# Performance work log

Measured on AMD Instinct MI355X. Metric: run time of the kernel, lower is better.

The kernel has to match this reference:

```python
import jax, jax.numpy as jnp
import numpy as np

D_MODEL = 1024
NHEAD = 8
DPH = D_MODEL // NHEAD
DFF = 2048
EPS = 1e-5


def _layernorm(x, w, b):
    mu = jnp.mean(x, axis=-1, keepdims=True)
    var = jnp.mean((x - mu) ** 2, axis=-1, keepdims=True)
    return (x - mu) / jnp.sqrt(var + EPS) * w + b


def setup_inputs() -> dict:
    key = jax.random.key(0)
    ks = jax.random.split(key, 8)
    B, L = 8, 2048
    x = jax.random.normal(ks[0], (B, L, D_MODEL), dtype=jnp.float32)
    # HeadWiseLinear: per-head weight (nhead, dph, 4*dph), bias (nhead, 4*dph)
    ih_w = jax.random.normal(ks[1], (NHEAD, DPH, 4 * DPH), dtype=jnp.float32) * (1.0 / np.sqrt(DPH))
    # forget-gate bias init: linspace(3,6,d_model) in the f slot (second chunk), zeros elsewhere
    init_vals = jnp.linspace(3.0, 6.0, D_MODEL, dtype=jnp.float32).reshape(NHEAD, 1, DPH)
    init_vals = jnp.pad(init_vals, ((0, 0), (1, 2), (0, 0)))  # rows: i, f, z, o
    ih_b = init_vals.reshape(NHEAD, 4 * DPH)
    # linear_hh: Linear(dph, 4*dph, bias=False), stored as (dph, 4*dph) (x @ W)
    hh_w = jax.random.normal(ks[2], (DPH, 4 * DPH), dtype=jnp.float32) * (1.0 / np.sqrt(DPH))
    ln1_w = jnp.ones((D_MODEL,), jnp.float32); ln1_b = jnp.zeros((D_MODEL,), jnp.float32)
    ln2_w = jnp.ones((D_MODEL,), jnp.float32); ln2_b = jnp.zeros((D_MODEL,), jnp.float32)
    hn_w = jnp.ones((DPH,), jnp.float32); hn_b = jnp.zeros((DPH,), jnp.float32)
    ff_w1 = jax.random.normal(ks[3], (D_MODEL, 2 * DFF), dtype=jnp.float32) * (1.0 / np.sqrt(D_MODEL))
    ff_b1 = jnp.zeros((2 * DFF,), jnp.float32)
    ff_w2 = jax.random.normal(ks[4], (DFF, D_MODEL), dtype=jnp.float32) * (1.0 / np.sqrt(DFF))
    ff_b2 = jnp.zeros((D_MODEL,), jnp.float32)
    return dict(x=x, ih_w=ih_w, ih_b=ih_b, hh_w=hh_w, ln1_w=ln1_w, ln1_b=ln1_b,
                hn_w=hn_w, hn_b=hn_b, ln2_w=ln2_w, ln2_b=ln2_b,
                ff_w1=ff_w1, ff_b1=ff_b1, ff_w2=ff_w2, ff_b2=ff_b2)


def _slstm_core(x, ih_w, ih_b, hh_w, hn_w, hn_b):
    B, L, D = x.shape
    xh = x.reshape(B, L, NHEAD, DPH)
    # headwise input projection: (B,L,H,4*dph)
    proj = jnp.einsum('blhd,hdf->blhf', xh, ih_w) + ih_b
    proj = jnp.transpose(proj, (1, 0, 2, 3))  # (L,B,H,4*dph)

    h0 = jnp.zeros((B, NHEAD, DPH), x.dtype)
    c0 = jnp.zeros_like(h0)
    m0 = jnp.full_like(h0, -jnp.inf)  # stabilizer; matches scalar-0 first-step semantics
    n0 = jnp.zeros_like(h0)

    def step(carry, p_t):
        h, c, m, n = carry
        p = p_t + jnp.einsum('bhd,df->bhf', h, hh_w)
        i, f, z, o = jnp.split(p, 4, axis=-1)
        z = jnp.tanh(z)
        o = jax.nn.sigmoid(o)
        f = jax.nn.log_sigmoid(f) + m
        m_new = jnp.maximum(f, i)
        i_s = jnp.exp(i - m_new)
        f_s = jnp.exp(f - m_new)
        c = f_s * c + i_s * z
        n = f_s * n + i_s
        h = o * (c / n)
        return (h, c, m_new, n), h

    (h, c, _, _), out = jax.lax.scan(step, (h0, c0, m0, n0), proj)
    out = jnp.transpose(out, (1, 0, 2, 3))  # (B,L,H,dph)
    out = _layernorm(out, hn_w, hn_b)
    return out.reshape(B, L, D), (h, c)


def reference(x, ih_w, ih_b, hh_w, ln1_w, ln1_b, hn_w, hn_b, ln2_w, ln2_b,
              ff_w1, ff_b1, ff_w2, ff_b2):
    core_out, _ = _slstm_core(_layernorm(x, ln1_w, ln1_b), ih_w, ih_b, hh_w, hn_w, hn_b)
    y = core_out + x
    z = _layernorm(y, ln2_w, ln2_b)
    x12 = z @ ff_w1 + ff_b1
    x1, x2 = jnp.split(x12, 2, axis=-1)
    ff = (x1 * jax.nn.gelu(x2, approximate=False)) @ ff_w2 + ff_b2
    return ff + y
```

## Files before the change

### kernel.cpp

```cpp
#include <hip/hip_runtime.h>
#include <math.h>


#define D_MODEL 1024
#define NHEAD   8
#define DPH     128
#define DFF     2048
#define BATCH   8
#define SEQ     2048
#define NROWS   (BATCH * SEQ)
#define CHUNK_L 256
#define TGRP    16
#define NGRP    (CHUNK_L / TGRP)
#define ROWCH   4096
#define LN_EPS  1e-5f

typedef __attribute__((ext_vector_type(8))) short short8;
typedef __attribute__((ext_vector_type(4))) short short4v;
typedef __attribute__((ext_vector_type(4))) float f32x4;
typedef __attribute__((ext_vector_type(2))) _Float16 h2f;
typedef __attribute__((ext_vector_type(8))) _Float16 h8f;
union H8U { h8f v; h2f p[4]; };

#if __has_builtin(__builtin_amdgcn_fdot2)
#define DOT2(a, b, c) __builtin_amdgcn_fdot2((a), (b), (c), false)
#else
__device__ __forceinline__ float DOT2(h2f a, h2f b, float c) {
  return c + (float)a.x * (float)b.x + (float)a.y * (float)b.y;
}
#endif

#if __has_builtin(__builtin_amdgcn_rcpf)
#define FRCP(x) __builtin_amdgcn_rcpf(x)
#else
#define FRCP(x) (1.0f / (x))
#endif

__device__ __forceinline__ float qxor1(float v) {
#if __has_builtin(__builtin_amdgcn_update_dpp)
  union { float f; int i; } u; u.f = v;
  u.i = __builtin_amdgcn_update_dpp(u.i, u.i, 0xB1, 0xf, 0xf, true);
  return u.f;
#else
  return __shfl_xor(v, 1, 64);
#endif
}
__device__ __forceinline__ float qxor2(float v) {
#if __has_builtin(__builtin_amdgcn_update_dpp)
  union { float f; int i; } u; u.f = v;
  u.i = __builtin_amdgcn_update_dpp(u.i, u.i, 0x4E, 0xf, 0xf, true);
  return u.f;
#else
  return __shfl_xor(v, 2, 64);
#endif
}

__device__ __forceinline__ void gll16(const void* src, void* lds_base, int lane) {
#if __has_builtin(__builtin_amdgcn_global_load_lds)
  __builtin_amdgcn_global_load_lds(
      (const __attribute__((address_space(1))) unsigned int*)src,
      (__attribute__((address_space(3))) unsigned int*)lds_base, 16, 0, 0);
#else
  *(float4*)((char*)lds_base + lane * 16) = *(const float4*)src;
#endif
}

__device__ __forceinline__ float gelu_exact(float x) {
  return 0.5f * x * (1.0f + erff(x * 0.70710678118654752440f));
}

__device__ __forceinline__ unsigned short f2bf(float f) {
  union { float f; unsigned int u; } v; v.f = f;
  unsigned int r = v.u + 0x7fffu + ((v.u >> 16) & 1u);
  return (unsigned short)(r >> 16);
}

__device__ __forceinline__ int img_off(int r, int k) {
  return r * 64 + ((((k >> 3) & 7) ^ (r & 7)) << 3) + (k & 7);
}

__device__ __forceinline__ float gate_step(float iv, float fv, float zraw, float oraw,
                                           float& c, float& nrm, float& m) {
  const float zv = 1.0f - 2.0f * FRCP(__expf(2.0f * zraw) + 1.0f);
  const float ov = FRCP(1.0f + __expf(-oraw));
  const float lf = fminf(fv, 0.0f) - __logf(1.0f + __expf(-fabsf(fv)));
  const float ft = lf + m;
  const float mn = fmaxf(ft, iv);
  const float is = __expf(iv - mn);
  const float fs = __expf(ft - mn);
  c = fs * c + is * zv;
  nrm = fs * nrm + is;
  m = mn;
  return ov * c * FRCP(nrm);
}

__global__ __launch_bounds__(256) void ln_stats_kernel(
    const float* __restrict__ in, float* __restrict__ mu_out,
    float* __restrict__ rs_out) {
  const int row = blockIdx.x, tid = threadIdx.x;
  const float4 v = ((const float4*)(in + (size_t)row * D_MODEL))[tid];
  float s  = v.x + v.y + v.z + v.w;
  float s2 = v.x*v.x + v.y*v.y + v.z*v.z + v.w*v.w;
  #pragma unroll
  for (int m = 1; m < 64; m <<= 1) { s += __shfl_xor(s, m, 64); s2 += __shfl_xor(s2, m, 64); }
  __shared__ float sa[4], sb[4];
  if ((tid & 63) == 0) { sa[tid >> 6] = s; sb[tid >> 6] = s2; }
  __syncthreads();
  if (tid == 0) {
    const float S  = sa[0] + sa[1] + sa[2] + sa[3];
    const float S2 = sb[0] + sb[1] + sb[2] + sb[3];
    const float mu = S * (1.0f / D_MODEL);
    const float var = S2 * (1.0f / D_MODEL) - mu * mu;
    mu_out[row] = mu;
    rs_out[row] = rsqrtf(var + LN_EPS);
  }
}

__global__ __launch_bounds__(256) void cvt_w(
    const float* __restrict__ src, short* __restrict__ dst, int K, int N) {
  __shared__ float tile[64][68];
  const int n0 = blockIdx.x * 64;
  const int k0 = blockIdx.y * 64;
  const int tid = threadIdx.x;
  #pragma unroll
  for (int i = 0; i < 16; ++i) {
    const int e = i * 256 + tid;
    const int kk = e >> 6, nn = e & 63;
    tile[kk][nn] = src[(size_t)(k0 + kk) * N + n0 + nn];
  }
  __syncthreads();
  const int ktiles = K >> 6;
  #pragma unroll
  for (int i = 0; i < 2; ++i) {
    const int e = i * 256 + tid;
    const int nn = e >> 3, kc = (e & 7) * 8;
    short8 s;
    #pragma unroll
    for (int j = 0; j < 8; ++j) s[j] = (short)f2bf(tile[kc + j][nn]);
    const int n = n0 + nn;
    const size_t base = ((size_t)(n >> 7) * ktiles + (k0 >> 6)) * 8192;
    *(short8*)(dst + base + img_off(n & 127, kc)) = s;
  }
}

__global__ __launch_bounds__(256) void cvt_hh(
    const float* __restrict__ hhw, h2f* __restrict__ hh2) {
  const int idx = blockIdx.x * 256 + threadIdx.x;
  const int k2 = idx >> 9, j = idx & 511;
  h2f v;
  v.x = (_Float16)hhw[(size_t)(2 * k2) * 512 + j];
  v.y = (_Float16)hhw[(size_t)(2 * k2 + 1) * 512 + j];
  hh2[idx] = v;
}

__global__ __launch_bounds__(256) void proj_gemm(
    const float* __restrict__ x, const float* __restrict__ mu1,
    const float* __restrict__ rs1, const float* __restrict__ ln1w,
    const float* __restrict__ ln1b, const float* __restrict__ ihw,
    const float* __restrict__ ihb, float* __restrict__ proj, int l0) {
  __shared__ __align__(16) float As[64][68];
  __shared__ __align__(16) float Bs[64][128];
  const int h  = blockIdx.z;
  const int qb = blockIdx.y;
  const int n0 = qb * 128;
  const int m0 = blockIdx.x * 64;
  const int tid = threadIdx.x;
  const int tm = (tid >> 5) << 3;
  const int tn = (tid & 31) << 2;
  float acc[8][4] = {};
  const float* Bb = ihw + (size_t)h * DPH * 512;
  for (int k0 = 0; k0 < DPH; k0 += 64) {
    #pragma unroll
    for (int i = 0; i < 4; ++i) {
      int idx = tid + i * 256;
      int r = idx >> 4, kk = (idx & 15) << 2;
      const int rowm = m0 + r;
      const int l = l0 + (rowm >> 3), b = rowm & 7;
      const int grow = b * SEQ + l;
      const float4 v = *(const float4*)(x + (size_t)grow * D_MODEL + h * DPH + k0 + kk);
      const float mu = mu1[grow], rs = rs1[grow];
      const float4 wv = *(const float4*)(ln1w + h * DPH + k0 + kk);
      const float4 bv = *(const float4*)(ln1b + h * DPH + k0 + kk);
      float4 o;
      o.x = (v.x - mu) * rs * wv.x + bv.x;
      o.y = (v.y - mu) * rs * wv.y + bv.y;
      o.z = (v.z - mu) * rs * wv.z + bv.z;
      o.w = (v.w - mu) * rs * wv.w + bv.w;
      *(float4*)&As[r][kk] = o;
    }
    #pragma unroll
    for (int i = 0; i < 8; ++i) {
      int idx = tid + i * 256;
      int kk = idx >> 5, nn = (idx & 31) << 2;
      *(float4*)&Bs[kk][nn] = *(const float4*)(Bb + (size_t)(k0 + kk) * 512 + n0 + nn);
    }
    __syncthreads();
    #pragma unroll 4
    for (int kk = 0; kk < 64; ++kk) {
      float a[8];
      #pragma unroll
      for (int i = 0; i < 8; ++i) a[i] = As[tm + i][kk];
      const float4 bv = *(const float4*)&Bs[kk][tn];
      #pragma unroll
      for (int i = 0; i < 8; ++i) {
        acc[i][0] += a[i] * bv.x; acc[i][1] += a[i] * bv.y;
        acc[i][2] += a[i] * bv.z; acc[i][3] += a[i] * bv.w;
      }
    }
    __syncthreads();
  }
  const float4 bias = *(const float4*)(ihb + h * 512 + n0 + tn);
  const int pos = n0 + ((tn + 8 * qb) & 127);
  #pragma unroll
  for (int i = 0; i < 8; ++i) {
    const int rowm = m0 + tm + i;
    float4 o;
    o.x = acc[i][0] + bias.x; o.y = acc[i][1] + bias.y;
    o.z = acc[i][2] + bias.z; o.w = acc[i][3] + bias.w;
    *(float4*)(proj + ((size_t)rowm * NHEAD + h) * 512 + pos) = o;
  }
}

__global__ __launch_bounds__(512, 1) void scan_chunk(
    const float* __restrict__ proj, const h2f* __restrict__ hh2,
    float* __restrict__ state, float* __restrict__ hout, int l0) {
  const int bh = blockIdx.x, b = bh >> 3, h = bh & 7;
  const int tid = threadIdx.x;
  const int l = tid & 63, w = tid >> 6;
  const int q = l & 3, p = l >> 2;
  const int ch = 16 * w + p;
  const int pvoff = q * 128 + ((ch + 8 * q) & 127);
  __shared__ __align__(16) _Float16 h16[2][128];
  __shared__ __align__(16) float pbuf[2][TGRP][512];
  __shared__ __align__(16) float hstage[2][TGRP][128];

  h2f w2[4][16];
  #pragma unroll
  for (int j = 0; j < 4; ++j)
    #pragma unroll
    for (int kk = 0; kk < 16; ++kk)
      w2[j][kk] = hh2[(size_t)(16 * q + kk) * 512 + j * 128 + ch];

  float c, nrm, m;
  if (l0 == 0) {
    c = 0.0f; nrm = 0.0f; m = -1e30f;
    if (q == 0) h16[0][ch] = (_Float16)0.0f;
  } else {
    c   = state[bh * 128 + ch];
    nrm = state[8192  + bh * 128 + ch];
    m   = state[16384 + bh * 128 + ch];
    if (q == 0) h16[0][ch] = (_Float16)state[24576 + bh * 128 + ch];
  }

  const float* pbase = proj + (size_t)bh * 512;

  #define STAGE(NB, GR)                                                        \
    {                                                                          \
      _Pragma("unroll")                                                        \
      for (int i = 0; i < 4; ++i) {                                            \
        const int hr = i * 8 + w;                                              \
        const float* src = pbase + (size_t)((GR) * TGRP + (hr >> 1)) * 32768   \
                           + (hr & 1) * 256 + l * 4;                           \
        float* dst = &pbuf[NB][0][0] + hr * 256;                               \
        gll16(src, dst, l);                                                    \
      }                                                                        \
    }

  STAGE(0, 0)
  asm volatile("s_waitcnt vmcnt(0)" ::: "memory");
  __syncthreads();

  float hv = 0.0f;
  for (int grp = 0; grp < NGRP; ++grp) {
    const int gb = grp & 1;
    if (grp + 1 < NGRP) STAGE(gb ^ 1, grp + 1)
    #pragma unroll
    for (int tl = 0; tl < TGRP; ++tl) {
      const int cur = tl & 1;
      float pa0 = 0.0f, pa1 = 0.0f, pa2 = 0.0f, pa3 = 0.0f;
      {
        const h8f* hp = (const h8f*)&h16[cur][q * 32];
        #pragma unroll
        for (int i = 0; i < 4; ++i) {
          H8U u; u.v = hp[i];
          #pragma unroll
          for (int e = 0; e < 4; ++e) {
            const int kk = i * 4 + e;
            pa0 = DOT2(u.p[e], w2[0][kk], pa0);
            pa1 = DOT2(u.p[e], w2[1][kk], pa1);
            pa2 = DOT2(u.p[e], w2[2][kk], pa2);
            pa3 = DOT2(u.p[e], w2[3][kk], pa3);
          }
        }
      }
      const float pv = pbuf[gb][tl][pvoff];
      pa0 += (q == 0) ? pv : 0.0f;
      pa1 += (q == 1) ? pv : 0.0f;
      pa2 += (q == 2) ? pv : 0.0f;
      pa3 += (q == 3) ? pv : 0.0f;
      pa0 += qxor1(pa0); pa1 += qxor1(pa1); pa2 += qxor1(pa2); pa3 += qxor1(pa3);
      pa0 += qxor2(pa0); pa1 += qxor2(pa1); pa2 += qxor2(pa2); pa3 += qxor2(pa3);
      hv = gate_step(pa0, pa1, pa2, pa3, c, nrm, m);
      if (q == 0) {
        h16[cur ^ 1][ch] = (_Float16)hv;
        hstage[gb][tl][ch] = hv;
      }
      __syncthreads();
    }
    {
      const int s = tid >> 5, c8 = (tid & 31) << 2;
      const float4 v0 = *(const float4*)&hstage[gb][s][c8];
      *(float4*)(hout + ((size_t)(b * SEQ + l0 + grp * TGRP + s)) * D_MODEL
                 + h * DPH + c8) = v0;
    }
  }

  if (q == 0) {
    state[bh * 128 + ch]          = c;
    state[8192  + bh * 128 + ch]  = nrm;
    state[16384 + bh * 128 + ch]  = m;
    state[24576 + bh * 128 + ch]  = hv;
  }
  #undef STAGE
}

__global__ __launch_bounds__(256) void post_kernel(
    float* __restrict__ yio, const float* __restrict__ x,
    const float* __restrict__ hnw, const float* __restrict__ hnb,
    float* __restrict__ mu2, float* __restrict__ rs2) {
  const int row = blockIdx.x, tid = threadIdx.x;
  const float4 hv = ((const float4*)(yio + (size_t)row * D_MODEL))[tid];
  float s  = hv.x + hv.y + hv.z + hv.w;
  float s2 = hv.x*hv.x + hv.y*hv.y + hv.z*hv.z + hv.w*hv.w;
  #pragma unroll
  for (int mm = 1; mm < 32; mm <<= 1) {
    s  += __shfl_xor(s,  mm, 32);
    s2 += __shfl_xor(s2, mm, 32);
  }
  const float mu = s * (1.0f / DPH);
  const float var = s2 * (1.0f / DPH) - mu * mu;
  const float rstd = rsqrtf(var + LN_EPS);
  const int dq = tid & 31;
  const float4 w4 = ((const float4*)hnw)[dq];
  const float4 b4 = ((const float4*)hnb)[dq];
  const float4 xv = ((const float4*)(x + (size_t)row * D_MODEL))[tid];
  float4 yv;
  yv.x = (hv.x - mu) * rstd * w4.x + b4.x + xv.x;
  yv.y = (hv.y - mu) * rstd * w4.y + b4.y + xv.y;
  yv.z = (hv.z - mu) * rstd * w4.z + b4.z + xv.z;
  yv.w = (hv.w - mu) * rstd * w4.w + b4.w + xv.w;
  ((float4*)(yio + (size_t)row * D_MODEL))[tid] = yv;
  float t1 = yv.x + yv.y + yv.z + yv.w;
  float t2 = yv.x*yv.x + yv.y*yv.y + yv.z*yv.z + yv.w*yv.w;
  #pragma unroll
  for (int mm = 1; mm < 64; mm <<= 1) {
    t1 += __shfl_xor(t1, mm, 64);
    t2 += __shfl_xor(t2, mm, 64);
  }
  __shared__ float sa[4], sb[4];
  if ((tid & 63) == 0) { sa[tid >> 6] = t1; sb[tid >> 6] = t2; }
  __syncthreads();
  if (tid == 0) {
    const float S  = sa[0] + sa[1] + sa[2] + sa[3];
    const float S2 = sb[0] + sb[1] + sb[2] + sb[3];
    const float m2 = S * (1.0f / D_MODEL);
    const float v2 = S2 * (1.0f / D_MODEL) - m2 * m2;
    mu2[row] = m2;
    rs2[row] = rsqrtf(v2 + LN_EPS);
  }
}

__global__ __launch_bounds__(256) void cvt_z(
    const float* __restrict__ y, const float* __restrict__ mu2,
    const float* __restrict__ rs2, const float* __restrict__ ln2w,
    const float* __restrict__ ln2b, short* __restrict__ zb, int row0) {
  const int lrow = blockIdx.x, tid = threadIdx.x;
  const int grow = row0 + lrow;
  const float4 v = ((const float4*)(y + (size_t)grow * D_MODEL))[tid];
  const float mu = mu2[grow], rs = rs2[grow];
  const float4 w4 = ((const float4*)ln2w)[tid];
  const float4 b4 = ((const float4*)ln2b)[tid];
  short4v s;
  s[0] = (short)f2bf((v.x - mu) * rs * w4.x + b4.x);
  s[1] = (short)f2bf((v.y - mu) * rs * w4.y + b4.y);
  s[2] = (short)f2bf((v.z - mu) * rs * w4.z + b4.z);
  s[3] = (short)f2bf((v.w - mu) * rs * w4.w + b4.w);
  const int k = tid * 4;
  const size_t base = ((size_t)(lrow >> 7) * 16 + (k >> 6)) * 8192;
  *(short4v*)(zb + base + img_off(lrow & 127, k & 63)) = s;
}

__global__ __launch_bounds__(256) void ff1_gemm(
    const short* __restrict__ zb, const short* __restrict__ w1b,
    const float* __restrict__ b1, short* __restrict__ g) {
  __shared__ short As[128 * 64];
  __shared__ short Bs1[128 * 64];
  __shared__ short Bs2[128 * 64];
  const int tid = threadIdx.x;
  const int mb = blockIdx.x;
  const int nb = blockIdx.y;
  const int lane = tid & 63;
  const int w = tid >> 6;
  const int wid = tid >> 6, wr = wid >> 1, wc = wid & 1;
  const short* at = zb + (size_t)mb * 16 * 8192;
  const short* b1t = w1b + (size_t)nb * 16 * 8192;
  const short* b2t = w1b + (size_t)(16 + nb) * 16 * 8192;
  f32x4 acc1[4][4], acc2[4][4];
  #pragma unroll
  for (int i = 0; i < 4; ++i)
    #pragma unroll
    for (int j = 0; j < 4; ++j) { acc1[i][j] = (f32x4)0.0f; acc2[i][j] = (f32x4)0.0f; }
  for (int kb = 0; kb < 16; ++kb) {
    #pragma unroll
    for (int i = 0; i < 4; ++i) {
      const int off = i * 2048 + w * 512;
      gll16(at + (size_t)kb * 8192 + off + lane * 8, As + off, lane);
      gll16(b1t + (size_t)kb * 8192 + off + lane * 8, Bs1 + off, lane);
      gll16(b2t + (size_t)kb * 8192 + off + lane * 8, Bs2 + off, lane);
    }
    __syncthreads();
    #pragma unroll
    for (int ks = 0; ks < 2; ++ks) {
      short8 af[4], b1f[4], b2f[4];
      #pragma unroll
      for (int mf = 0; mf < 4; ++mf) {
        const int row = wr * 64 + mf * 16 + (lane & 15);
        const int c8 = ks * 4 + (lane >> 4);
        af[mf] = *(const short8*)&As[row * 64 + ((c8 ^ (row & 7)) << 3)];
      }
      #pragma unroll
      for (int nf = 0; nf < 4; ++nf) {
        const int row = wc * 64 + nf * 16 + (lane & 15);
        const int c8 = ks * 4 + (lane >> 4);
        const int off = row * 64 + ((c8 ^ (row & 7)) << 3);
        b1f[nf] = *(const short8*)&Bs1[off];
        b2f[nf] = *(const short8*)&Bs2[off];
      }
      #pragma unroll
      for (int mf = 0; mf < 4; ++mf)
        #pragma unroll
        for (int nf = 0; nf < 4; ++nf) {
          acc1[mf][nf] = __builtin_amdgcn_mfma_f32_16x16x32_bf16(af[mf], b1f[nf], acc1[mf][nf], 0, 0, 0);
          acc2[mf][nf] = __builtin_amdgcn_mfma_f32_16x16x32_bf16(af[mf], b2f[nf], acc2[mf][nf], 0, 0, 0);
        }
    }
    __syncthreads();
  }
  #pragma unroll
  for (int nf = 0; nf < 4; ++nf) {
    const int col = nb * 128 + wc * 64 + nf * 16 + (lane & 15);
    const float bx1 = b1[col], bx2 = b1[DFF + col];
    #pragma unroll
    for (int mf = 0; mf < 4; ++mf) {
      const int rloc = wr * 64 + mf * 16 + ((lane >> 4) << 2);
      #pragma unroll
      for (int rr = 0; rr < 4; ++rr) {
        const float x1 = acc1[mf][nf][rr] + bx1;
        const float x2 = acc2[mf][nf][rr] + bx2;
        const int r = rloc + rr;
        const size_t base = ((size_t)mb * 32 + (col >> 6)) * 8192;
        g[base + img_off(r, col & 63)] = (short)f2bf(x1 * gelu_exact(x2));
      }
    }
  }
}

__global__ __launch_bounds__(256) void ff2_gemm(
    const short* __restrict__ g, const short* __restrict__ w2b,
    const float* __restrict__ b2, float* __restrict__ out, int row0) {
  __shared__ short As[128 * 64];
  __shared__ short Bs[128 * 64];
  const int tid = threadIdx.x;
  const int mb = blockIdx.x;
  const int nb = blockIdx.y;
  const int lane = tid & 63;
  const int w = tid >> 6;
  const int wid = tid >> 6, wr = wid >> 1, wc = wid & 1;
  const short* at = g + (size_t)mb * 32 * 8192;
  const short* bt = w2b + (size_t)nb * 32 * 8192;
  f32x4 acc[4][4];
  #pragma unroll
  for (int i = 0; i < 4; ++i)
    #pragma unroll
    for (int j = 0; j < 4; ++j) acc[i][j] = (f32x4)0.0f;
  for (int kb = 0; kb < 32; ++kb) {
    #pragma unroll
    for (int i = 0; i < 4; ++i) {
      const int off = i * 2048 + w * 512;
      gll16(at + (size_t)kb * 8192 + off + lane * 8, As + off, lane);
      gll16(bt + (size_t)kb * 8192 + off + lane * 8, Bs + off, lane);
    }
    __syncthreads();
    #pragma unroll
    for (int ks = 0; ks < 2; ++ks) {
      short8 af[4], bf[4];
      #pragma unroll
      for (int mf = 0; mf < 4; ++mf) {
        const int row = wr * 64 + mf * 16 + (lane & 15);
        const int c8 = ks * 4 + (lane >> 4);
        af[mf] = *(const short8*)&As[row * 64 + ((c8 ^ (row & 7)) << 3)];
      }
      #pragma unroll
      for (int nf = 0; nf < 4; ++nf) {
        const int row = wc * 64 + nf * 16 + (lane & 15);
        const int c8 = ks * 4 + (lane >> 4);
        bf[nf] = *(const short8*)&Bs[row * 64 + ((c8 ^ (row & 7)) << 3)];
      }
      #pragma unroll
      for (int mf = 0; mf < 4; ++mf)
        #pragma unroll
        for (int nf = 0; nf < 4; ++nf)
          acc[mf][nf] = __builtin_amdgcn_mfma_f32_16x16x32_bf16(af[mf], bf[nf], acc[mf][nf], 0, 0, 0);
    }
    __syncthreads();
  }
  #pragma unroll
  for (int nf = 0; nf < 4; ++nf) {
    const int col = nb * 128 + wc * 64 + nf * 16 + (lane & 15);
    const float bias = b2[col];
    #pragma unroll
    for (int mf = 0; mf < 4; ++mf) {
      const int rbase = row0 + mb * 128 + wr * 64 + mf * 16 + ((lane >> 4) << 2);
      #pragma unroll
      for (int rr = 0; rr < 4; ++rr) {
        float* p = out + (size_t)(rbase + rr) * D_MODEL + col;
        *p = acc[mf][nf][rr] + bias + *p;
      }
    }
  }
}

extern "C" void kernel_launch(void* const* d_in, const int* in_sizes, int n_in,
                              void* d_out, int out_size, void* d_ws, size_t ws_size,
                              hipStream_t stream) {
  const float* x    = (const float*)d_in[0];
  const float* ihw  = (const float*)d_in[1];
  const float* ihb  = (const float*)d_in[2];
  const float* hhw  = (const float*)d_in[3];
  const float* ln1w = (const float*)d_in[4];
  const float* ln1b = (const float*)d_in[5];
  const float* hnw  = (const float*)d_in[6];
  const float* hnb  = (const float*)d_in[7];
  const float* ln2w = (const float*)d_in[8];
  const float* ln2b = (const float*)d_in[9];
  const float* ffw1 = (const float*)d_in[10];
  const float* ffb1 = (const float*)d_in[11];
  const float* ffw2 = (const float*)d_in[12];
  const float* ffb2 = (const float*)d_in[13];

  float* ws    = (float*)d_ws;
  float* r0    = ws;
  float* state = ws + 8388608;
  float* mu1   = ws + 8421376;
  float* rs1   = ws + 8437760;
  float* mu2   = ws + 8454144;
  float* rs2   = ws + 8470528;
  short* w1b   = (short*)(ws + 8486912);
  short* w2b   = (short*)(ws + 10584064);
  h2f*   hh2   = (h2f*)(ws + 11632640);
  short* gb    = (short*)r0;
  short* zb    = (short*)(ws + 4194304);
  float* out   = (float*)d_out;

  cvt_w<<<dim3(4096 / 64, 1024 / 64), 256, 0, stream>>>(ffw1, w1b, 1024, 4096);
  cvt_w<<<dim3(1024 / 64, 2048 / 64), 256, 0, stream>>>(ffw2, w2b, 2048, 1024);
  cvt_hh<<<128, 256, 0, stream>>>(hhw, hh2);
  ln_stats_kernel<<<NROWS, 256, 0, stream>>>(x, mu1, rs1);
  for (int cidx = 0; cidx < SEQ / CHUNK_L; ++cidx) {
    const int l0 = cidx * CHUNK_L;
    proj_gemm<<<dim3(CHUNK_L * BATCH / 64, 512 / 128, NHEAD), 256, 0, stream>>>(
        x, mu1, rs1, ln1w, ln1b, ihw, ihb, r0, l0);
    scan_chunk<<<BATCH * NHEAD, 512, 0, stream>>>(r0, hh2, state, out, l0);
  }
  post_kernel<<<NROWS, 256, 0, stream>>>(out, x, hnw, hnb, mu2, rs2);
  for (int rc = 0; rc < NROWS / ROWCH; ++rc) {
    const int row0 = rc * ROWCH;
    cvt_z<<<ROWCH, 256, 0, stream>>>(out, mu2, rs2, ln2w, ln2b, zb, row0);
    ff1_gemm<<<dim3(ROWCH / 128, DFF / 128), 256, 0, stream>>>(zb, w1b, ffb1, gb);
    ff2_gemm<<<dim3(ROWCH / 128, D_MODEL / 128), 256, 0, stream>>>(
        gb, w2b, ffb2, out, row0);
  }
}
```

Before: 2.023 ms.

## Move headwise input projection to bf16 MFMA with a pre-normalized swizzled input

The fp32 SIMT projection GEMM is replaced by two steps. A cvt_x kernel applies LayerNorm1 and writes bf16 tiles in the swizzled image layout, and a proj_mfma kernel uses 16x16x32 bf16 MFMA instructions with the per-head input weights converted to bf16. The gate step also computes only one exp instead of two, since one of the two stabilized exponents is always exp(0). This cuts the arithmetic cost of the projection but adds an extra kernel launch and a bf16 round trip per chunk, and lowers precision of the projection inputs.

```diff
diff --git a/kernel.cpp b/kernel.cpp
--- a/kernel.cpp
+++ b/kernel.cpp
@@ -86,8 +86,9 @@
   const float lf = fminf(fv, 0.0f) - __logf(1.0f + __expf(-fabsf(fv)));
   const float ft = lf + m;
   const float mn = fmaxf(ft, iv);
-  const float is = __expf(iv - mn);
-  const float fs = __expf(ft - mn);
+  const float e  = __expf(fminf(ft, iv) - mn);
+  const float is = (iv < ft) ? e : 1.0f;
+  const float fs = (iv < ft) ? 1.0f : e;
   c = fs * c + is * zv;
   nrm = fs * nrm + is;
   m = mn;
@@ -153,71 +154,91 @@
   hh2[idx] = v;
 }
 
-__global__ __launch_bounds__(256) void proj_gemm(
+__global__ __launch_bounds__(256) void cvt_x(
     const float* __restrict__ x, const float* __restrict__ mu1,
     const float* __restrict__ rs1, const float* __restrict__ ln1w,
-    const float* __restrict__ ln1b, const float* __restrict__ ihw,
-    const float* __restrict__ ihb, float* __restrict__ proj, int l0) {
-  __shared__ __align__(16) float As[64][68];
-  __shared__ __align__(16) float Bs[64][128];
+    const float* __restrict__ ln1b, short* __restrict__ xb, int l0) {
+  const int rowm = blockIdx.x, tid = threadIdx.x;
+  const int l = l0 + (rowm >> 3), b = rowm & 7;
+  const int grow = b * SEQ + l;
+  const float4 v = ((const float4*)(x + (size_t)grow * D_MODEL))[tid];
+  const float mu = mu1[grow], rs = rs1[grow];
+  const float4 w4 = ((const float4*)ln1w)[tid];
+  const float4 b4 = ((const float4*)ln1b)[tid];
+  short4v s;
+  s[0] = (short)f2bf((v.x - mu) * rs * w4.x + b4.x);
+  s[1] = (short)f2bf((v.y - mu) * rs * w4.y + b4.y);
+  s[2] = (short)f2bf((v.z - mu) * rs * w4.z + b4.z);
+  s[3] = (short)f2bf((v.w - mu) * rs * w4.w + b4.w);
+  const int k = tid * 4;
+  const int h = k >> 7, khead = k & 127;
+  const size_t base = (((size_t)(rowm >> 7) * 8 + h) * 2 + (khead >> 6)) * 8192;
+  *(short4v*)(xb + base + img_off(rowm & 127, khead & 63)) = s;
+}
+
+__global__ __launch_bounds__(256) void proj_mfma(
+    const short* __restrict__ xb, const short* __restrict__ ihwb,
+    const float* __restrict__ ihb, float* __restrict__ proj) {
+  __shared__ short As[128 * 64];
+  __shared__ short Bs[128 * 64];
+  const int tid = threadIdx.x;
+  const int mb = blockIdx.x;
+  const int qb = blockIdx.y;
   const int h  = blockIdx.z;
-  const int qb = blockIdx.y;
-  const int n0 = qb * 128;
-  const int m0 = blockIdx.x * 64;
-  const int tid = threadIdx.x;
-  const int tm = (tid >> 5) << 3;
-  const int tn = (tid & 31) << 2;
-  float acc[8][4] = {};
-  const float* Bb = ihw + (size_t)h * DPH * 512;
-  for (int k0 = 0; k0 < DPH; k0 += 64) {
+  const int lane = tid & 63;
+  const int w = tid >> 6;
+  const int wr = w >> 1, wc = w & 1;
+  const short* at = xb + ((size_t)(mb * 8 + h) * 2) * 8192;
+  const short* bt = ihwb + ((size_t)(h * 8 + qb * 2)) * 8192;
+  f32x4 acc[4][4];
+  #pragma unroll
+  for (int i = 0; i < 4; ++i)
+    #pragma unroll
+    for (int j = 0; j < 4; ++j) acc[i][j] = (f32x4)0.0f;
+  #pragma unroll
+  for (int kb = 0; kb < 2; ++kb) {
     #pragma unroll
     for (int i = 0; i < 4; ++i) {
-      int idx = tid + i * 256;
-      int r = idx >> 4, kk = (idx & 15) << 2;
-      const int rowm = m0 + r;
-      const int l = l0 + (rowm >> 3), b = rowm & 7;
-      const int grow = b * SEQ + l;
-      const float4 v = *(const float4*)(x + (size_t)grow * D_MODEL + h * DPH + k0 + kk);
-      const float mu = mu1[grow], rs = rs1[grow];
-      const float4 wv = *(const float4*)(ln1w + h * DPH + k0 + kk);
-      const float4 bv = *(const float4*)(ln1b + h * DPH + k0 + kk);
-      float4 o;
-      o.x = (v.x - mu) * rs * wv.x + bv.x;
-      o.y = (v.y - mu) * rs * wv.y + bv.y;
-      o.z = (v.z - mu) * rs * wv.z + bv.z;
-      o.w = (v.w - mu) * rs * wv.w + bv.w;
-      *(float4*)&As[r][kk] = o;
-    }
-    #pragma unroll
-    for (int i = 0; i < 8; ++i) {
-      int idx = tid + i * 256;
-      int kk = idx >> 5, nn = (idx & 31) << 2;
-      *(float4*)&Bs[kk][nn] = *(const float4*)(Bb + (size_t)(k0 + kk) * 512 + n0 + nn);
+      const int off = i * 2048 + w * 512;
+      gll16(at + (size_t)kb * 8192 + off + lane * 8, As + off, lane);
+      gll16(bt + (size_t)kb * 8192 + off + lane * 8, Bs + off, lane);
     }
     __syncthreads();
-    #pragma unroll 4
-    for (int kk = 0; kk < 64; ++kk) {
-      float a[8];
-      #pragma unroll
-      for (int i = 0; i < 8; ++i) a[i] = As[tm + i][kk];
-      const float4 bv = *(const float4*)&Bs[kk][tn];
-      #pragma unroll
-      for (int i = 0; i < 8; ++i) {
-        acc[i][0] += a[i] * bv.x; acc[i][1] += a[i] * bv.y;
-        acc[i][2] += a[i] * bv.z; acc[i][3] += a[i] * bv.w;
-      }
+    #pragma unroll
+    for (int ks = 0; ks < 2; ++ks) {
+      short8 af[4], bf[4];
+      #pragma unroll
+      for (int mf = 0; mf < 4; ++mf) {
+        const int row = wr * 64 + mf * 16 + (lane & 15);
+        const int c8 = ks * 4 + (lane >> 4);
+        af[mf] = *(const short8*)&As[row * 64 + ((c8 ^ (row & 7)) << 3)];
+      }
+      #pragma unroll
+      for (int nf = 0; nf < 4; ++nf) {
+        const int row = wc * 64 + nf * 16 + (lane & 15);
+        const int c8 = ks * 4 + (lane >> 4);
+        bf[nf] = *(const short8*)&Bs[row * 64 + ((c8 ^ (row & 7)) << 3)];
+      }
+      #pragma unroll
+      for (int mf = 0; mf < 4; ++mf)
+        #pragma unroll
+        for (int nf = 0; nf < 4; ++nf)
+          acc[mf][nf] = __builtin_amdgcn_mfma_f32_16x16x32_bf16(af[mf], bf[nf], acc[mf][nf], 0, 0, 0);
     }
     __syncthreads();
   }
-  const float4 bias = *(const float4*)(ihb + h * 512 + n0 + tn);
-  const int pos = n0 + ((tn + 8 * qb) & 127);
-  #pragma unroll
-  for (int i = 0; i < 8; ++i) {
-    const int rowm = m0 + tm + i;
-    float4 o;
-    o.x = acc[i][0] + bias.x; o.y = acc[i][1] + bias.y;
-    o.z = acc[i][2] + bias.z; o.w = acc[i][3] + bias.w;
-    *(float4*)(proj + ((size_t)rowm * NHEAD + h) * 512 + pos) = o;
+  #pragma unroll
+  for (int nf = 0; nf < 4; ++nf) {
+    const int col = wc * 64 + nf * 16 + (lane & 15);
+    const float bias = ihb[h * 512 + qb * 128 + col];
+    const int pos = qb * 128 + ((col + 8 * qb) & 127);
+    #pragma unroll
+    for (int mf = 0; mf < 4; ++mf) {
+      const int rbase = mb * 128 + wr * 64 + mf * 16 + ((lane >> 4) << 2);
+      #pragma unroll
+      for (int rr = 0; rr < 4; ++rr)
+        proj[((size_t)(rbase + rr) * NHEAD + h) * 512 + pos] = acc[mf][nf][rr] + bias;
+    }
   }
 }
 
@@ -401,7 +422,7 @@
   const int nb = blockIdx.y;
   const int lane = tid & 63;
   const int w = tid >> 6;
-  const int wid = tid >> 6, wr = wid >> 1, wc = wid & 1;
+  const int wr = w >> 1, wc = w & 1;
   const short* at = zb + (size_t)mb * 16 * 8192;
   const short* b1t = w1b + (size_t)nb * 16 * 8192;
   const short* b2t = w1b + (size_t)(16 + nb) * 16 * 8192;
@@ -475,7 +496,7 @@
   const int nb = blockIdx.y;
   const int lane = tid & 63;
   const int w = tid >> 6;
-  const int wid = tid >> 6, wr = wid >> 1, wc = wid & 1;
+  const int wr = w >> 1, wc = w & 1;
   const short* at = g + (size_t)mb * 32 * 8192;
   const short* bt = w2b + (size_t)nb * 32 * 8192;
   f32x4 acc[4][4];
@@ -558,18 +579,23 @@
   short* w1b   = (short*)(ws + 8486912);
   short* w2b   = (short*)(ws + 10584064);
   h2f*   hh2   = (h2f*)(ws + 11632640);
+  short* xb    = (short*)(ws + 11665408);
+  short* ihwb  = (short*)(ws + 12713984);
   short* gb    = (short*)r0;
   short* zb    = (short*)(ws + 4194304);
   float* out   = (float*)d_out;
 
   cvt_w<<<dim3(4096 / 64, 1024 / 64), 256, 0, stream>>>(ffw1, w1b, 1024, 4096);
   cvt_w<<<dim3(1024 / 64, 2048 / 64), 256, 0, stream>>>(ffw2, w2b, 2048, 1024);
+  for (int h = 0; h < NHEAD; ++h)
+    cvt_w<<<dim3(8, 2), 256, 0, stream>>>(ihw + (size_t)h * 65536,
+                                          ihwb + (size_t)h * 8 * 8192, 128, 512);
   cvt_hh<<<128, 256, 0, stream>>>(hhw, hh2);
   ln_stats_kernel<<<NROWS, 256, 0, stream>>>(x, mu1, rs1);
   for (int cidx = 0; cidx < SEQ / CHUNK_L; ++cidx) {
     const int l0 = cidx * CHUNK_L;
-    proj_gemm<<<dim3(CHUNK_L * BATCH / 64, 512 / 128, NHEAD), 256, 0, stream>>>(
-        x, mu1, rs1, ln1w, ln1b, ihw, ihb, r0, l0);
+    cvt_x<<<CHUNK_L * BATCH, 256, 0, stream>>>(x, mu1, rs1, ln1w, ln1b, xb, l0);
+    proj_mfma<<<dim3(16, 4, NHEAD), 256, 0, stream>>>(xb, ihwb, ihb, r0);
     scan_chunk<<<BATCH * NHEAD, 512, 0, stream>>>(r0, hh2, state, out, l0);
   }
   post_kernel<<<NROWS, 256, 0, stream>>>(out, x, hnw, hnb, mu2, rs2);
```

After: 1.953 ms. -3.5%, faster.
